# Kernel tuning notes

Hardware: AMD Instinct MI355X
Metric: run time of the kernel (lower is better)

Reference implementation:

```python
import jax, jax.numpy as jnp
import numpy as np

LAMDA = 0.5  # weight between agent-selected hidden state and current hidden state
SAMPLE_SEED = 42  # RNG for categorical action sampling (torch version is stochastic)


def setup_inputs() -> dict:
    B, T, D, H, U, A = 256, 512, 128, 128, 64, 10
    key = jax.random.key(0)
    ks = jax.random.split(key, 16)
    s = 0.1
    return {
        "x": jax.random.normal(ks[0], (B, T, D), dtype=jnp.float32),
        "mask": jnp.ones((B, T), dtype=jnp.int32),
        # GRUCell params (torch layout: [3H, in], gate order r,z,n)
        "gru_w_ih": jax.random.normal(ks[1], (3 * H, D), dtype=jnp.float32) * s,
        "gru_w_hh": jax.random.normal(ks[2], (3 * H, H), dtype=jnp.float32) * s,
        "gru_b_ih": jnp.zeros((3 * H,), dtype=jnp.float32),
        "gru_b_hh": jnp.zeros((3 * H,), dtype=jnp.float32),
        # agent1 MLP: observes mean of hidden buffer ([B,H])
        "a1_w1": jax.random.normal(ks[3], (U, H), dtype=jnp.float32) * s,
        "a1_b1": jnp.zeros((U,), dtype=jnp.float32),
        "a1_w2": jax.random.normal(ks[4], (A, U), dtype=jnp.float32) * s,
        "a1_b2": jnp.zeros((A,), dtype=jnp.float32),
        # agent2 MLP: observes current input ([B,D])
        "a2_w1": jax.random.normal(ks[5], (U, D), dtype=jnp.float32) * s,
        "a2_b1": jnp.zeros((U,), dtype=jnp.float32),
        "a2_w2": jax.random.normal(ks[6], (A, U), dtype=jnp.float32) * s,
        "a2_b2": jnp.zeros((A,), dtype=jnp.float32),
    }


def _gru_cell(xt, h, w_ih, w_hh, b_ih, b_hh):
    gi = xt @ w_ih.T + b_ih  # [B, 3H]
    gh = h @ w_hh.T + b_hh
    ir, iz, inn = jnp.split(gi, 3, axis=-1)
    hr, hz, hn = jnp.split(gh, 3, axis=-1)
    r = jax.nn.sigmoid(ir + hr)
    z = jax.nn.sigmoid(iz + hz)
    n = jnp.tanh(inn + r * hn)
    return (1.0 - z) * n + z * h


def _agent_action(obs, w1, b1, w2, b2, key):
    # observation is detached in the original (choose_action detaches)
    z = jnp.tanh(jax.lax.stop_gradient(obs) @ w1.T + b1)
    logits = z @ w2.T + b2  # Categorical(softmax(logits)) == categorical over logits
    return jax.random.categorical(key, logits, axis=-1)  # [B]


def reference(x, mask, gru_w_ih, gru_w_hh, gru_b_ih, gru_b_hh,
              a1_w1, a1_b1, a1_w2, a1_b2, a2_w1, a2_b1, a2_w2, a2_b2):
    B, T, D = x.shape
    H = gru_w_hh.shape[1]
    A = a1_w2.shape[0]
    keys = jax.random.split(jax.random.key(SAMPLE_SEED), 2 * T).reshape(T, 2)

    gru = lambda xt, h: _gru_cell(xt, h, gru_w_ih, gru_w_hh, gru_b_ih, gru_b_hh)

    # t == 0: cur_h is zeros, action_h == cur_h, so weighted_h == 0; agent samples
    # at t=0 are discarded for state (they only fill RL bookkeeping lists).
    h0 = gru(x[:, 0], jnp.zeros((B, H), x.dtype))
    buf0 = jnp.zeros((A, B, H), x.dtype)  # observed_h history buffer
    bidx = jnp.arange(B)

    def step(carry, inp):
        h, buf = carry
        xt, kt = inp
        buf = jnp.concatenate([buf[1:], h[None]], axis=0)  # shift in previous hidden
        a1 = _agent_action(buf.mean(axis=0), a1_w1, a1_b1, a1_w2, a1_b2, kt[0])
        a2 = _agent_action(xt, a2_w1, a2_b1, a2_w2, a2_b2, kt[1])
        action_h = (buf[a1, bidx] + buf[a2, bidx]) * 0.5  # [B,H] gather of past states
        weighted_h = LAMDA * action_h + (1.0 - LAMDA) * h
        hn = gru(xt, weighted_h)
        return (hn, buf), hn

    xs = (jnp.swapaxes(x[:, 1:], 0, 1), keys[1:])  # time-major
    _, hs = jax.lax.scan(step, (h0, buf0), xs)
    h_all = jnp.swapaxes(jnp.concatenate([h0[None], hs], axis=0), 0, 1)  # [B,T,H]

    last_idx = jnp.sum(mask, axis=1) - 1  # get_last_visit
    last_out = h_all[bidx, last_idx]  # [B,H]; dropout=0.0 -> identity
    return last_out, h_all
```

## Files before the change

### kernel.cpp

```cpp
#include <hip/hip_runtime.h>
#include <math.h>

#define B_ 256
#define T_ 512
#define D_ 128
#define H_ 128
#define BH_ 32768
#define NG 1308160

__device__ __forceinline__ void bar_lds() {
  asm volatile("s_waitcnt lgkmcnt(0)\n\ts_barrier" ::: "memory");
}

__device__ __forceinline__ float dpp_add_xor1(float v) {
  int r = __builtin_amdgcn_update_dpp(0, __float_as_int(v), 0xB1, 0xF, 0xF, true);
  return v + __int_as_float(r);
}
__device__ __forceinline__ float dpp_add_xor2(float v) {
  int r = __builtin_amdgcn_update_dpp(0, __float_as_int(v), 0x4E, 0xF, 0xF, true);
  return v + __int_as_float(r);
}

__device__ __forceinline__ float frcp(float x) { return __builtin_amdgcn_rcpf(x); }
__device__ __forceinline__ float fsigmoid(float x) { return frcp(1.0f + __expf(-x)); }
__device__ __forceinline__ float ftanh_(float x) { return 1.0f - 2.0f * frcp(1.0f + __expf(2.0f * x)); }

__device__ __forceinline__ void tf2x32(unsigned k0, unsigned k1, unsigned x0, unsigned x1,
                                       unsigned& o0, unsigned& o1) {
  unsigned k2 = k0 ^ k1 ^ 0x1BD11BDAu;
  unsigned v0 = x0 + k0, v1 = x1 + k1;
#define TFR(r) { v0 += v1; v1 = (v1 << (r)) | (v1 >> (32 - (r))); v1 ^= v0; }
  TFR(13) TFR(15) TFR(26) TFR(6)   v0 += k1; v1 += k2 + 1u;
  TFR(17) TFR(29) TFR(16) TFR(24)  v0 += k2; v1 += k0 + 2u;
  TFR(13) TFR(15) TFR(26) TFR(6)   v0 += k0; v1 += k1 + 3u;
  TFR(17) TFR(29) TFR(16) TFR(24)  v0 += k1; v1 += k2 + 4u;
  TFR(13) TFR(15) TFR(26) TFR(6)   v0 += k2; v1 += k0 + 5u;
#undef TFR
  o0 = v0; o1 = v1;
}

__device__ __forceinline__ float gumbel_f(unsigned bits) {
  const float tiny = 1.17549435e-38f;
  float u = __uint_as_float((bits >> 9) | 0x3f800000u) - 1.0f;
  u = u + tiny;
  u = fmaxf(tiny, u);
  return -__logf(-__logf(u));
}

__global__ void p0_keys(unsigned* __restrict__ keys_tab) {
  int i = blockIdx.x * blockDim.x + threadIdx.x;
  if (i >= 1024) return;
  unsigned o0, o1;
  tf2x32(0u, 42u, 0u, (unsigned)i, o0, o1);
  keys_tab[2 * i] = o0; keys_tab[2 * i + 1] = o1;
}

#define SX 264
#define SW 72
__global__ __launch_bounds__(256, 4) void gemm_tiled(
    const float* __restrict__ x, const float* __restrict__ w_ih,
    const float* __restrict__ b_ih, const float* __restrict__ a2w1,
    const float* __restrict__ a2b1, float* __restrict__ gi, float* __restrict__ zt) {
  __shared__ __align__(16) float Xs[32 * SX];
  __shared__ __align__(16) float Ws[32 * SW];
  const int tid = threadIdx.x;
  const int mb = blockIdx.x & 511;
  const int nb = blockIdx.x >> 9;
  const bool isz = (nb == 6);
  const size_t m0 = (size_t)mb * 256;
  const int n0 = isz ? 0 : nb * 64;
  const float* wsrc = isz ? a2w1 : w_ih;
  const float* bsrc = isz ? a2b1 : b_ih;
  const int mt = tid >> 4;
  const int nt = tid & 15;
  const int kg = tid >> 5;
  const int ri = tid & 31;

  float acc[16][4];
  #pragma unroll
  for (int i = 0; i < 16; i++)
    #pragma unroll
    for (int j = 0; j < 4; j++) acc[i][j] = 0.f;

  #pragma unroll 1
  for (int kc = 0; kc < 4; kc++) {
    const int k0 = kc * 32;
    __syncthreads();
    #pragma unroll
    for (int p = 0; p < 8; p++) {
      int row = ri + 32 * p;
      float4 v = *(const float4*)(x + (m0 + row) * 128 + k0 + 4 * kg);
      Xs[(4 * kg + 0) * SX + row] = v.x;
      Xs[(4 * kg + 1) * SX + row] = v.y;
      Xs[(4 * kg + 2) * SX + row] = v.z;
      Xs[(4 * kg + 3) * SX + row] = v.w;
    }
    #pragma unroll
    for (int p = 0; p < 2; p++) {
      int n = ri + 32 * p;
      float4 v = *(const float4*)(wsrc + (size_t)(n0 + n) * 128 + k0 + 4 * kg);
      Ws[(4 * kg + 0) * SW + n] = v.x;
      Ws[(4 * kg + 1) * SW + n] = v.y;
      Ws[(4 * kg + 2) * SW + n] = v.z;
      Ws[(4 * kg + 3) * SW + n] = v.w;
    }
    __syncthreads();
    #pragma unroll 4
    for (int kk = 0; kk < 32; kk++) {
      const float* xrow = Xs + kk * SX + mt * 16;
      float4 xa0 = ((const float4*)xrow)[0];
      float4 xa1 = ((const float4*)xrow)[1];
      float4 xa2 = ((const float4*)xrow)[2];
      float4 xa3 = ((const float4*)xrow)[3];
      float4 wv = *(const float4*)(Ws + kk * SW + nt * 4);
      float xv[16] = {xa0.x, xa0.y, xa0.z, xa0.w, xa1.x, xa1.y, xa1.z, xa1.w,
                      xa2.x, xa2.y, xa2.z, xa2.w, xa3.x, xa3.y, xa3.z, xa3.w};
      #pragma unroll
      for (int i = 0; i < 16; i++) {
        acc[i][0] += xv[i] * wv.x;
        acc[i][1] += xv[i] * wv.y;
        acc[i][2] += xv[i] * wv.z;
        acc[i][3] += xv[i] * wv.w;
      }
    }
  }
  float4 bias = *(const float4*)(bsrc + n0 + nt * 4);
  if (!isz) {
    #pragma unroll
    for (int i = 0; i < 16; i++) {
      float4 o;
      o.x = acc[i][0] + bias.x; o.y = acc[i][1] + bias.y;
      o.z = acc[i][2] + bias.z; o.w = acc[i][3] + bias.w;
      size_t m = m0 + (size_t)mt * 16 + i;
      *(float4*)(gi + m * 384 + n0 + nt * 4) = o;
    }
  } else {
    #pragma unroll
    for (int i = 0; i < 16; i++) {
      float4 o;
      o.x = ftanh_(acc[i][0] + bias.x); o.y = ftanh_(acc[i][1] + bias.y);
      o.z = ftanh_(acc[i][2] + bias.z); o.w = ftanh_(acc[i][3] + bias.w);
      size_t m = m0 + (size_t)mt * 16 + i;
      *(float4*)(zt + m * 64 + nt * 4) = o;
    }
  }
}

__global__ __launch_bounds__(256) void sampler(
    const float* __restrict__ zt, const float* __restrict__ w2,
    const float* __restrict__ b2, const unsigned* __restrict__ keys_tab,
    float* __restrict__ g1, int* __restrict__ a2_tab) {
  __shared__ __align__(16) float w2s[10][68];
  __shared__ float b2s[10];
  __shared__ __align__(16) float zs[4][64];
  const int tid = threadIdx.x, w = tid >> 6, lane = tid & 63;
  const int t = blockIdx.x + 1;
  for (int i = tid; i < 640; i += 256) w2s[i >> 6][i & 63] = w2[i];
  if (tid < 10) b2s[tid] = b2[tid];
  __syncthreads();
  const unsigned k0a = keys_tab[2 * (2 * t + 1)], k1a = keys_tab[2 * (2 * t + 1) + 1];
  const unsigned k0g = keys_tab[2 * (2 * t)],     k1g = keys_tab[2 * (2 * t) + 1];
  const int a = lane & 15, kc = lane >> 4;
  float zr = zt[((size_t)w * 512 + t) * 64 + lane];
  #pragma unroll 1
  for (int it = 0; it < 64; it++) {
    const int b = 4 * it + w;
    zs[w][lane] = zr;
    if (it < 63) zr = zt[((size_t)(b + 4) * 512 + t) * 64 + lane];
    float p = 0.f;
    if (a < 10) {
      const float4* zp = (const float4*)(&zs[w][16 * kc]);
      const float4* wp = (const float4*)(&w2s[a][16 * kc]);
      #pragma unroll
      for (int c = 0; c < 4; c++) {
        float4 zv = zp[c], w4 = wp[c];
        p += w4.x * zv.x + w4.y * zv.y + w4.z * zv.z + w4.w * zv.w;
      }
    }
    p += __shfl_xor(p, 16);
    p += __shfl_xor(p, 32);
    float val = -3.0e38f;
    if (a < 10 && kc == 0) {
      unsigned o0, o1;
      tf2x32(k0a, k1a, 0u, (unsigned)(b * 10 + a), o0, o1);
      val = (p + b2s[a]) + gumbel_f(o0 ^ o1);
      tf2x32(k0g, k1g, 0u, (unsigned)(b * 10 + a), o0, o1);
      g1[((size_t)(t - 1) * 256 + b) * 10 + a] = gumbel_f(o0 ^ o1);
    }
    float best = 0.f; int bi = 0;
    #pragma unroll
    for (int aa = 0; aa < 10; aa++) {
      float v = __shfl(val, aa);
      if (aa == 0 || v > best) { best = v; bi = aa; }
    }
    if (lane == 0) a2_tab[(size_t)(t - 1) * 256 + b] = bi;
  }
}

__global__ __launch_bounds__(512, 2) void seq_kernel(
    const float* __restrict__ gi_glob, const int* __restrict__ mask,
    const float* __restrict__ w_hh, const float* __restrict__ b_hh,
    const float* __restrict__ a1w1, const float* __restrict__ a1b1,
    const float* __restrict__ a1w2, const float* __restrict__ a1b2,
    const float* __restrict__ g1_tab, const int* __restrict__ a2_tab,
    float* __restrict__ out) {
  __shared__ __align__(16) float ring2[20][128];
  __shared__ __align__(16) float yc[10][384];
  __shared__ __align__(16) float hbuf[128];
  __shared__ __align__(16) float ghi[384];
  __shared__ __align__(16) float obs[128];
  __shared__ __align__(16) float osum[128];
  __shared__ __align__(16) float z1buf[64];
  __shared__ __align__(16) float lastbuf[128];
  __shared__ __align__(16) float w2buf[10][68];
  __shared__ float bhh3s[128];
  __shared__ float b1s[64], b2s[10];
  __shared__ float g1buf[10];
  __shared__ float2 pl2[16];
  __shared__ int a2s_lds;
  __shared__ int redi[8];
  __shared__ int last_s;

  const int tid = threadIdx.x;
  const int wave = tid >> 6, lane = tid & 63;
  const int b = blockIdx.x;

  float4 wr[4][8];
  const int q = tid >> 2, qk = tid & 3;
  if (tid < 384) {
    #pragma unroll
    for (int i = 0; i < 4; i++) {
      const float* basep = w_hh + (size_t)(4 * q + i) * 128 + 4 * qk;
      #pragma unroll
      for (int c = 0; c < 8; c++) wr[i][c] = *(const float4*)(basep + 16 * c);
    }
  }
  float4 w1reg[16];
  float4 bhh4a = make_float4(0.f, 0.f, 0.f, 0.f);
  if (wave >= 6) {
    int m = ((wave - 6) << 5) + (lane >> 1);
    int kc = lane & 1;
    const float4* wp = (const float4*)(a1w1 + (size_t)m * 128 + 64 * kc);
    #pragma unroll
    for (int c = 0; c < 16; c++) w1reg[c] = wp[c];
  }
  if (wave == 6) bhh4a = ((const float4*)b_hh)[lane];

  for (int idx = tid; idx < 2560; idx += 512) ((float*)ring2)[idx] = 0.f;
  for (int idx = tid; idx < 3840; idx += 512) ((float*)yc)[idx] = 0.f;
  for (int idx = tid; idx < 640; idx += 512) w2buf[idx >> 6][idx & 63] = a1w2[idx];
  if (tid < 128) bhh3s[tid] = b_hh[256 + tid];
  if (tid < 64) b1s[tid] = a1b1[tid];
  if (tid < 10) b2s[tid] = a1b2[tid];
  int mv = mask[(size_t)b * T_ + tid];
  #pragma unroll
  for (int off = 1; off < 64; off <<= 1) mv += __shfl_xor(mv, off);
  if (lane == 0) redi[wave] = mv;
  const float4* gi4 = (const float4*)gi_glob;
  float4 gir0 = make_float4(0.f, 0.f, 0.f, 0.f), gir1 = gir0;
  if (wave == 6) {
    size_t base1 = ((size_t)b * 512 + 1) * 96;
    gir0 = gi4[base1 + lane];
    if (lane < 32) gir1 = gi4[base1 + 64 + lane];
  }
  float g1r = 0.f; int a2r = 0;
  if (wave == 7 && lane < 10) g1r = g1_tab[(size_t)b * 10 + lane];
  if (wave == 7 && lane == 12) a2r = a2_tab[b];
  __syncthreads();
  if (tid == 0) {
    int s = 0;
    #pragma unroll
    for (int w = 0; w < 8; w++) s += redi[w];
    last_s = s - 1;
  }
  __syncthreads();
  const int last = last_s;

  if (tid < 128) {
    int j = tid;
    const float* g0 = gi_glob + (size_t)b * 512 * 384;
    float r  = fsigmoid(g0[j] + b_hh[j]);
    float zz = fsigmoid(g0[128 + j] + b_hh[128 + j]);
    float n  = ftanh_(g0[256 + j] + r * b_hh[256 + j]);
    float hnew = (1.0f - zz) * n;
    hbuf[j] = hnew; ring2[0][j] = hnew; ring2[10][j] = hnew;
    obs[j] = hnew / 10.0f;
    out[BH_ + ((size_t)b * 512) * 128 + j] = hnew;
    if (0 == last) lastbuf[j] = hnew;
  }
  __syncthreads();

  #pragma unroll 1
  for (int t = 1; t < T_; t++) {
    const int sn = (t + 9) % 10;
    if (tid < 384) {
      const float4* hb4 = (const float4*)hbuf;
      float4 a0 = make_float4(0.f, 0.f, 0.f, 0.f), a1v = a0, a2v = a0, a3v = a0;
      #pragma unroll
      for (int c = 0; c < 8; c++) {
        float4 h4 = hb4[4 * c + qk];
        a0.x += wr[0][c].x * h4.x; a0.y += wr[0][c].y * h4.y; a0.z += wr[0][c].z * h4.z; a0.w += wr[0][c].w * h4.w;
        a1v.x += wr[1][c].x * h4.x; a1v.y += wr[1][c].y * h4.y; a1v.z += wr[1][c].z * h4.z; a1v.w += wr[1][c].w * h4.w;
        a2v.x += wr[2][c].x * h4.x; a2v.y += wr[2][c].y * h4.y; a2v.z += wr[2][c].z * h4.z; a2v.w += wr[2][c].w * h4.w;
        a3v.x += wr[3][c].x * h4.x; a3v.y += wr[3][c].y * h4.y; a3v.z += wr[3][c].z * h4.z; a3v.w += wr[3][c].w * h4.w;
      }
      float s0  = (a0.x + a0.y) + (a0.z + a0.w);
      float s1v = (a1v.x + a1v.y) + (a1v.z + a1v.w);
      float s2v = (a2v.x + a2v.y) + (a2v.z + a2v.w);
      float s3v = (a3v.x + a3v.y) + (a3v.z + a3v.w);
      s0  = dpp_add_xor2(dpp_add_xor1(s0));
      s1v = dpp_add_xor2(dpp_add_xor1(s1v));
      s2v = dpp_add_xor2(dpp_add_xor1(s2v));
      s3v = dpp_add_xor2(dpp_add_xor1(s3v));
      float my = (qk == 0) ? s0 : (qk == 1) ? s1v : (qk == 2) ? s2v : s3v;
      yc[sn][4 * q + qk] = my;
      if (tid >= 128 && tid < 256) {
        int j = tid - 128;
        int bs = (t + 1) % 10;
        float s = 0.f;
        #pragma unroll
        for (int a = 0; a < 9; a++) s += ring2[bs + a][j];
        osum[j] = s;
      }
    } else if (wave == 6) {
      float4 g0 = gir0;
      g0.x += bhh4a.x; g0.y += bhh4a.y; g0.z += bhh4a.z; g0.w += bhh4a.w;
      ((float4*)ghi)[lane] = g0;
      if (lane < 32) ((float4*)ghi)[64 + lane] = gir1;
      if (t < 511) {
        size_t basep = ((size_t)b * 512 + t + 1) * 96;
        gir0 = gi4[basep + lane];
        if (lane < 32) gir1 = gi4[basep + 64 + lane];
      }
      {
        int m = lane >> 1, kc = lane & 1;
        float ax = 0.f, ay = 0.f, az = 0.f, aw = 0.f;
        #pragma unroll
        for (int c = 0; c < 16; c++) {
          float4 o4 = ((const float4*)obs)[16 * kc + c];
          ax += w1reg[c].x * o4.x; ay += w1reg[c].y * o4.y;
          az += w1reg[c].z * o4.z; aw += w1reg[c].w * o4.w;
        }
        float d = (ax + ay) + (az + aw);
        d = dpp_add_xor1(d);
        if (kc == 0) z1buf[m] = ftanh_(d + b1s[m]);
      }
      if (lane < 40) {
        int a = lane >> 2, k2 = lane & 3;
        int m0 = 8 * k2;
        float4 z4a = ((const float4*)(z1buf + m0))[0], z4b = ((const float4*)(z1buf + m0))[1];
        float4 wa = ((const float4*)(&w2buf[a][m0]))[0], wb = ((const float4*)(&w2buf[a][m0]))[1];
        float p = z4a.x * wa.x + z4a.y * wa.y + z4a.z * wa.z + z4a.w * wa.w
                + z4b.x * wb.x + z4b.y * wb.y + z4b.z * wb.z + z4b.w * wb.w;
        p = dpp_add_xor2(dpp_add_xor1(p));
        if (k2 == 0) pl2[a].x = p + b2s[a];
      }
    } else {
      if (lane < 10) g1buf[lane] = g1r;
      if (lane == 12) a2s_lds = a2r;
      if (t < 511) {
        if (lane < 10) g1r = g1_tab[((size_t)t * 256 + b) * 10 + lane];
        if (lane == 12) a2r = a2_tab[(size_t)t * 256 + b];
      }
      {
        int m = 32 + (lane >> 1), kc = lane & 1;
        float ax = 0.f, ay = 0.f, az = 0.f, aw = 0.f;
        #pragma unroll
        for (int c = 0; c < 16; c++) {
          float4 o4 = ((const float4*)obs)[16 * kc + c];
          ax += w1reg[c].x * o4.x; ay += w1reg[c].y * o4.y;
          az += w1reg[c].z * o4.z; aw += w1reg[c].w * o4.w;
        }
        float d = (ax + ay) + (az + aw);
        d = dpp_add_xor1(d);
        if (kc == 0) z1buf[m] = ftanh_(d + b1s[m]);
      }
      if (lane < 40) {
        int a = lane >> 2, k2 = lane & 3;
        int m0 = 32 + 8 * k2;
        float4 z4a = ((const float4*)(z1buf + m0))[0], z4b = ((const float4*)(z1buf + m0))[1];
        float4 wa = ((const float4*)(&w2buf[a][m0]))[0], wb = ((const float4*)(&w2buf[a][m0]))[1];
        float p = z4a.x * wa.x + z4a.y * wa.y + z4a.z * wa.z + z4a.w * wa.w
                + z4b.x * wb.x + z4b.y * wb.y + z4b.z * wb.z + z4b.w * wb.w;
        p = dpp_add_xor2(dpp_add_xor1(p));
        if (k2 == 0) pl2[a].y = p + g1buf[a];
      }
    }
    bar_lds();

    if (tid < 128) {
      float best = 0.f; int bi = 0;
      #pragma unroll
      for (int a = 0; a < 10; a++) {
        float2 pv = pl2[a];
        float v = pv.x + pv.y;
        if (a == 0 || v > best) { best = v; bi = a; }
      }
      const int s1 = (t + bi) % 10;
      const int s2 = (t + a2s_lds) % 10;
      int j = tid;
      float gh1 = 0.5f * (0.5f * (yc[s1][j]       + yc[s2][j]))       + 0.5f * yc[sn][j];
      float gh2 = 0.5f * (0.5f * (yc[s1][128 + j] + yc[s2][128 + j])) + 0.5f * yc[sn][128 + j];
      float gh3 = bhh3s[j] + 0.5f * (0.5f * (yc[s1][256 + j] + yc[s2][256 + j])) + 0.5f * yc[sn][256 + j];
      float r  = fsigmoid(ghi[j] + gh1);
      float zz = fsigmoid(ghi[128 + j] + gh2);
      float n  = ftanh_(ghi[256 + j] + r * gh3);
      float hw = 0.5f * ((ring2[s1][j] + ring2[s2][j]) * 0.5f) + 0.5f * hbuf[j];
      float hnew = (1.0f - zz) * n + zz * hw;
      hbuf[j] = hnew;
      ring2[t % 10][j] = hnew;
      ring2[t % 10 + 10][j] = hnew;
      out[BH_ + ((size_t)b * 512 + t) * 128 + j] = hnew;
      if (t == last) lastbuf[j] = hnew;
      obs[j] = (osum[j] + hnew) / 10.0f;
    }
    bar_lds();
  }
  if (tid < 128) out[(size_t)b * H_ + tid] = lastbuf[tid];
}

extern "C" void kernel_launch(void* const* d_in, const int* in_sizes, int n_in,
                              void* d_out, int out_size, void* d_ws, size_t ws_size,
                              hipStream_t stream) {
  (void)in_sizes; (void)n_in; (void)out_size; (void)ws_size;
  const float* x     = (const float*)d_in[0];
  const int*   mask  = (const int*)d_in[1];
  const float* w_ih  = (const float*)d_in[2];
  const float* w_hh  = (const float*)d_in[3];
  const float* b_ih  = (const float*)d_in[4];
  const float* b_hh  = (const float*)d_in[5];
  const float* a1w1  = (const float*)d_in[6];
  const float* a1b1  = (const float*)d_in[7];
  const float* a1w2  = (const float*)d_in[8];
  const float* a1b2  = (const float*)d_in[9];
  const float* a2w1  = (const float*)d_in[10];
  const float* a2b1  = (const float*)d_in[11];
  const float* a2w2  = (const float*)d_in[12];
  const float* a2b2  = (const float*)d_in[13];
  float* out = (float*)d_out;

  float*    gi       = (float*)d_ws;
  float*    g1       = gi + (size_t)131072 * 384;
  unsigned* keys_tab = (unsigned*)(g1 + NG);
  int*      a2_tab   = (int*)(keys_tab + 2048);
  float*    zt       = (float*)(a2_tab + 130816);

  p0_keys<<<4, 256, 0, stream>>>(keys_tab);
  gemm_tiled<<<3584, 256, 0, stream>>>(x, w_ih, b_ih, a2w1, a2b1, gi, zt);
  sampler<<<511, 256, 0, stream>>>(zt, a2w2, a2b2, keys_tab, g1, a2_tab);
  seq_kernel<<<256, 512, 0, stream>>>(gi, mask, w_hh, b_hh,
                                      a1w1, a1b1, a1w2, a1b2, g1, a2_tab, out);
}
```

Measured before the change: 1.064 ms.

## Interleave per-slot gate partials and hidden state into float4 LDS records

Replaces the separate yc gate-partial array, ghi and ring2 reads in the serial gate update with interleaved slot records, so each thread fetches r/z/n partials plus the stored hidden state with one float4 LDS load per slot. The input gates are also packed with the n-bias as a float4 per element. Agent waves get raised scheduling priority, and output stores become nontemporal. This cuts LDS instruction count on the per-step critical path at the cost of a larger LDS footprint and an extra record write per step.

Measured after the change: 1.051 ms (median of 2 runs). No clear change (-1.3%).

```diff
diff --git a/kernel.cpp b/kernel.cpp
--- a/kernel.cpp
+++ b/kernel.cpp
@@ -205,15 +205,14 @@
     const float* __restrict__ g1_tab, const int* __restrict__ a2_tab,
     float* __restrict__ out) {
   __shared__ __align__(16) float ring2[20][128];
-  __shared__ __align__(16) float yc[10][384];
+  __shared__ __align__(16) float slotrec[10][512];
+  __shared__ __align__(16) float ghi4[512];
   __shared__ __align__(16) float hbuf[128];
-  __shared__ __align__(16) float ghi[384];
   __shared__ __align__(16) float obs[128];
   __shared__ __align__(16) float osum[128];
   __shared__ __align__(16) float z1buf[64];
   __shared__ __align__(16) float lastbuf[128];
   __shared__ __align__(16) float w2buf[10][68];
-  __shared__ float bhh3s[128];
   __shared__ float b1s[64], b2s[10];
   __shared__ float g1buf[10];
   __shared__ float2 pl2[16];
@@ -236,7 +235,6 @@
     }
   }
   float4 w1reg[16];
-  float4 bhh4a = make_float4(0.f, 0.f, 0.f, 0.f);
   if (wave >= 6) {
     int m = ((wave - 6) << 5) + (lane >> 1);
     int kc = lane & 1;
@@ -244,28 +242,28 @@
     #pragma unroll
     for (int c = 0; c < 16; c++) w1reg[c] = wp[c];
   }
-  if (wave == 6) bhh4a = ((const float4*)b_hh)[lane];
+  float bhh6[6] = {0.f, 0.f, 0.f, 0.f, 0.f, 0.f};
+  float gc[6] = {0.f, 0.f, 0.f, 0.f, 0.f, 0.f};
+  if (wave == 6) {
+    bhh6[0] = b_hh[lane];       bhh6[1] = b_hh[128 + lane]; bhh6[2] = b_hh[256 + lane];
+    bhh6[3] = b_hh[64 + lane];  bhh6[4] = b_hh[192 + lane]; bhh6[5] = b_hh[320 + lane];
+    const float* p1 = gi_glob + ((size_t)b * 512 + 1) * 384;
+    gc[0] = p1[lane];      gc[1] = p1[128 + lane]; gc[2] = p1[256 + lane];
+    gc[3] = p1[64 + lane]; gc[4] = p1[192 + lane]; gc[5] = p1[320 + lane];
+  }
+  float g1r = 0.f; int a2r = 0;
+  if (wave == 7 && lane < 10) g1r = g1_tab[(size_t)b * 10 + lane];
+  if (wave == 7 && lane == 12) a2r = a2_tab[b];
 
   for (int idx = tid; idx < 2560; idx += 512) ((float*)ring2)[idx] = 0.f;
-  for (int idx = tid; idx < 3840; idx += 512) ((float*)yc)[idx] = 0.f;
+  for (int idx = tid; idx < 5120; idx += 512) ((float*)slotrec)[idx] = 0.f;
   for (int idx = tid; idx < 640; idx += 512) w2buf[idx >> 6][idx & 63] = a1w2[idx];
-  if (tid < 128) bhh3s[tid] = b_hh[256 + tid];
   if (tid < 64) b1s[tid] = a1b1[tid];
   if (tid < 10) b2s[tid] = a1b2[tid];
   int mv = mask[(size_t)b * T_ + tid];
   #pragma unroll
   for (int off = 1; off < 64; off <<= 1) mv += __shfl_xor(mv, off);
   if (lane == 0) redi[wave] = mv;
-  const float4* gi4 = (const float4*)gi_glob;
-  float4 gir0 = make_float4(0.f, 0.f, 0.f, 0.f), gir1 = gir0;
-  if (wave == 6) {
-    size_t base1 = ((size_t)b * 512 + 1) * 96;
-    gir0 = gi4[base1 + lane];
-    if (lane < 32) gir1 = gi4[base1 + 64 + lane];
-  }
-  float g1r = 0.f; int a2r = 0;
-  if (wave == 7 && lane < 10) g1r = g1_tab[(size_t)b * 10 + lane];
-  if (wave == 7 && lane == 12) a2r = a2_tab[b];
   __syncthreads();
   if (tid == 0) {
     int s = 0;
@@ -284,8 +282,9 @@
     float n  = ftanh_(g0[256 + j] + r * b_hh[256 + j]);
     float hnew = (1.0f - zz) * n;
     hbuf[j] = hnew; ring2[0][j] = hnew; ring2[10][j] = hnew;
+    slotrec[0][(j << 2) + 3] = hnew;
     obs[j] = hnew / 10.0f;
-    out[BH_ + ((size_t)b * 512) * 128 + j] = hnew;
+    __builtin_nontemporal_store(hnew, &out[BH_ + ((size_t)b * 512) * 128 + j]);
     if (0 == last) lastbuf[j] = hnew;
   }
   __syncthreads();
@@ -313,7 +312,7 @@
       s2v = dpp_add_xor2(dpp_add_xor1(s2v));
       s3v = dpp_add_xor2(dpp_add_xor1(s3v));
       float my = (qk == 0) ? s0 : (qk == 1) ? s1v : (qk == 2) ? s2v : s3v;
-      yc[sn][4 * q + qk] = my;
+      slotrec[sn][((tid & 127) << 2) + (tid >> 7)] = my;
       if (tid >= 128 && tid < 256) {
         int j = tid - 128;
         int bs = (t + 1) % 10;
@@ -323,14 +322,17 @@
         osum[j] = s;
       }
     } else if (wave == 6) {
-      float4 g0 = gir0;
-      g0.x += bhh4a.x; g0.y += bhh4a.y; g0.z += bhh4a.z; g0.w += bhh4a.w;
-      ((float4*)ghi)[lane] = g0;
-      if (lane < 32) ((float4*)ghi)[64 + lane] = gir1;
+      __builtin_amdgcn_s_setprio(1);
+      float4 e0, e1;
+      e0.x = gc[0] + bhh6[0]; e0.y = gc[1] + bhh6[1]; e0.z = gc[2]; e0.w = bhh6[2];
+      e1.x = gc[3] + bhh6[3]; e1.y = gc[4] + bhh6[4]; e1.z = gc[5]; e1.w = bhh6[5];
+      ((float4*)ghi4)[lane] = e0;
+      ((float4*)ghi4)[64 + lane] = e1;
+      float gn0 = 0.f, gn1 = 0.f, gn2 = 0.f, gn3 = 0.f, gn4 = 0.f, gn5 = 0.f;
       if (t < 511) {
-        size_t basep = ((size_t)b * 512 + t + 1) * 96;
-        gir0 = gi4[basep + lane];
-        if (lane < 32) gir1 = gi4[basep + 64 + lane];
+        const float* bp = gi_glob + ((size_t)b * 512 + t + 1) * 384;
+        gn0 = bp[lane];      gn1 = bp[128 + lane]; gn2 = bp[256 + lane];
+        gn3 = bp[64 + lane]; gn4 = bp[192 + lane]; gn5 = bp[320 + lane];
       }
       {
         int m = lane >> 1, kc = lane & 1;
@@ -355,7 +357,10 @@
         p = dpp_add_xor2(dpp_add_xor1(p));
         if (k2 == 0) pl2[a].x = p + b2s[a];
       }
+      gc[0] = gn0; gc[1] = gn1; gc[2] = gn2; gc[3] = gn3; gc[4] = gn4; gc[5] = gn5;
+      __builtin_amdgcn_s_setprio(0);
     } else {
+      __builtin_amdgcn_s_setprio(1);
       if (lane < 10) g1buf[lane] = g1r;
       if (lane == 12) a2s_lds = a2r;
       if (t < 511) {
@@ -385,6 +390,7 @@
         p = dpp_add_xor2(dpp_add_xor1(p));
         if (k2 == 0) pl2[a].y = p + g1buf[a];
       }
+      __builtin_amdgcn_s_setprio(0);
     }
     bar_lds();
 
@@ -399,24 +405,29 @@
       const int s1 = (t + bi) % 10;
       const int s2 = (t + a2s_lds) % 10;
       int j = tid;
-      float gh1 = 0.5f * (0.5f * (yc[s1][j]       + yc[s2][j]))       + 0.5f * yc[sn][j];
-      float gh2 = 0.5f * (0.5f * (yc[s1][128 + j] + yc[s2][128 + j])) + 0.5f * yc[sn][128 + j];
-      float gh3 = bhh3s[j] + 0.5f * (0.5f * (yc[s1][256 + j] + yc[s2][256 + j])) + 0.5f * yc[sn][256 + j];
-      float r  = fsigmoid(ghi[j] + gh1);
-      float zz = fsigmoid(ghi[128 + j] + gh2);
-      float n  = ftanh_(ghi[256 + j] + r * gh3);
-      float hw = 0.5f * ((ring2[s1][j] + ring2[s2][j]) * 0.5f) + 0.5f * hbuf[j];
+      float4 y1 = *(const float4*)(&slotrec[s1][j << 2]);
+      float4 y2 = *(const float4*)(&slotrec[s2][j << 2]);
+      float4 yn = *(const float4*)(&slotrec[sn][j << 2]);
+      float4 gv = ((const float4*)ghi4)[j];
+      float gh1 = 0.5f * (0.5f * (y1.x + y2.x)) + 0.5f * yn.x;
+      float gh2 = 0.5f * (0.5f * (y1.y + y2.y)) + 0.5f * yn.y;
+      float gh3 = gv.w + 0.5f * (0.5f * (y1.z + y2.z)) + 0.5f * yn.z;
+      float r  = fsigmoid(gv.x + gh1);
+      float zz = fsigmoid(gv.y + gh2);
+      float n  = ftanh_(gv.z + r * gh3);
+      float hw = 0.5f * ((y1.w + y2.w) * 0.5f) + 0.5f * yn.w;
       float hnew = (1.0f - zz) * n + zz * hw;
       hbuf[j] = hnew;
       ring2[t % 10][j] = hnew;
       ring2[t % 10 + 10][j] = hnew;
-      out[BH_ + ((size_t)b * 512 + t) * 128 + j] = hnew;
+      slotrec[t % 10][(j << 2) + 3] = hnew;
+      __builtin_nontemporal_store(hnew, &out[BH_ + ((size_t)b * 512 + t) * 128 + j]);
       if (t == last) lastbuf[j] = hnew;
       obs[j] = (osum[j] + hnew) / 10.0f;
     }
     bar_lds();
   }
-  if (tid < 128) out[(size_t)b * H_ + tid] = lastbuf[tid];
+  if (tid < 128) __builtin_nontemporal_store(lastbuf[tid], &out[(size_t)b * H_ + tid]);
 }
 
 extern "C" void kernel_launch(void* const* d_in, const int* in_sizes, int n_in,
```
